# Performance work log

Measured on AMD Instinct MI355X. Metric: run time of the kernel, lower is better.

The kernel has to match this reference:

```python
import jax, jax.numpy as jnp
import numpy as np

# dims (see shape_source)
N, L = 64, 2048          # batch, signal length (l_in)
C1, C2, C3 = 64, 128, 256  # hidden_dims
LAT = 2 * C3             # latent dim: Linear maps L->2 per channel -> C3*2
LD = 64                  # decoder latent spatial length


def conv1d(x, W, b):
    # x: [N,C_in,L], W: [C_out,C_in,3], 'same' padding, stride 1
    y = jax.lax.conv_general_dilated(x, W, window_strides=(1,), padding=((1, 1),),
                                     dimension_numbers=('NCH', 'OIH', 'NCH'))
    return y + b[None, :, None]


def lrelu(v):
    return jnp.where(v > 0, v, 0.01 * v)  # LeakyReLU default slope


def setup_inputs() -> dict:
    key = jax.random.key(0)
    ks = jax.random.split(key, 24)
    r = lambda k, shape, s: (jax.random.normal(k, shape, dtype=jnp.float32) * s)
    inp = {}
    inp['x'] = jax.random.normal(ks[0], (N, 1, L), dtype=jnp.float32)
    # shared encoder (original code reuses the same `modules` for class & style encoders)
    inp['W1'] = r(ks[1], (C1, 1, 3), 0.3);   inp['b1'] = r(ks[2], (C1,), 0.05)
    inp['W2'] = r(ks[3], (C2, C1, 3), 0.08); inp['b2'] = r(ks[4], (C2,), 0.05)
    inp['W3'] = r(ks[5], (C3, C2, 3), 0.06); inp['b3'] = r(ks[6], (C3,), 0.05)
    # heads: Linear(L -> 2) applied on last dim. class_logvar reuses class_mu head (bug in original, kept).
    inp['cm_W'] = r(ks[7], (2, L), 0.02);  inp['cm_b'] = r(ks[8], (2,), 0.05)
    inp['sm_W'] = r(ks[9], (2, L), 0.02);  inp['sm_b'] = r(ks[10], (2,), 0.05)
    inp['sl_W'] = r(ks[11], (2, L), 0.02); inp['sl_b'] = r(ks[12], (2,), 0.05)
    # projections latent -> decoder feature map (minimal repair: original decoder cannot consume a vector)
    inp['pc_W'] = r(ks[13], (C3 * LD, LAT), 0.05); inp['pc_b'] = r(ks[14], (C3 * LD,), 0.05)
    inp['ps_W'] = r(ks[15], (C3 * LD, LAT), 0.05); inp['ps_b'] = r(ks[16], (C3 * LD,), 0.05)
    # shared decoder conv stack (original also shares `modules` between class & style decoders)
    inp['V1'] = r(ks[17], (C2, C3, 3), 0.06); inp['c1'] = r(ks[18], (C2,), 0.05)
    inp['V2'] = r(ks[19], (C1, C2, 3), 0.08); inp['c2'] = r(ks[20], (C1,), 0.05)
    # reparameterization noise (replaces torch.randn_like)
    inp['eps_c'] = jax.random.normal(ks[21], (LAT,), dtype=jnp.float32)
    inp['eps_s'] = jax.random.normal(ks[22], (N, LAT), dtype=jnp.float32)
    return inp


def reference(x, W1, b1, W2, b2, W3, b3, cm_W, cm_b, sm_W, sm_b, sl_W, sl_b,
              pc_W, pc_b, ps_W, ps_b, V1, c1, V2, c2, eps_c, eps_s):
    # ---- encode (shared encoder weights, as in the original module) ----
    h = lrelu(conv1d(x, W1, b1))
    h = lrelu(conv1d(h, W2, b2))
    h = lrelu(conv1d(h, W3, b3))                       # [N, C3, L]
    head = lambda W, b: (jnp.einsum('ncl,dl->ncd', h, W) + b[None, None, :]).reshape(N, -1)
    class_mu = head(cm_W, cm_b)                        # [N, LAT]
    class_logvar = class_mu                            # bug-faithful: class_logvar uses class_mu head
    style_mu = head(sm_W, sm_b)
    style_logvar = head(sl_W, sl_b)
    # ---- accumulate_group_evidence: precision-weighted Gaussian fusion over the batch ----
    prec = jnp.exp(-class_logvar)                      # 1/var, [N, LAT]
    group_var = 1.0 / jnp.sum(prec, axis=0)            # [LAT]
    group_mu = group_var * jnp.sum(class_mu * prec, axis=0)
    group_logvar = jnp.log(group_var)
    # ---- reparameterize ----
    z_c = eps_c * jnp.exp(0.5 * group_logvar) + group_mu       # [LAT]
    z_s = eps_s * jnp.exp(0.5 * style_logvar) + style_mu       # [N, LAT]
    # ---- decode ----
    content = (pc_W @ z_c + pc_b).reshape(1, C3, LD)
    d = jax.nn.relu(conv1d(content, V1, c1))
    d = jax.nn.relu(conv1d(d, V2, c2))                 # [1, C1, LD]
    source = jnp.mean(d, axis=0).reshape(-1)           # [C1*LD] fixed observation kernel
    m = (z_s @ ps_W.T + ps_b[None, :]).reshape(N, C3, LD)
    m = jax.nn.relu(conv1d(m, V1, c1))
    m = jax.nn.relu(conv1d(m, V2, c2)).reshape(N, -1)  # [N, C1*LD]
    # F.conv_transpose1d(media, source) with stride 1 == full 1D convolution
    out = jax.vmap(lambda mi: jnp.convolve(mi, source, mode='full'))(m)
    return out.reshape(N, 1, -1)                       # [N, 1, 2*C1*LD - 1]
```

## Files before the change

### kernel.cpp

```cpp
#include <hip/hip_runtime.h>
#include <math.h>


using short8  = __attribute__((ext_vector_type(8))) short;
using floatx4 = __attribute__((ext_vector_type(4))) float;

__device__ __forceinline__ float lrelu_s(float v, float slope) {
  return v > 0.f ? v : slope * v;
}
__device__ __forceinline__ unsigned short bf16_rne(float f) {
  unsigned u = __float_as_uint(f);
  u += 0x7FFFu + ((u >> 16) & 1u);
  return (unsigned short)(u >> 16);
}
__device__ __forceinline__ float bf16_to_f(unsigned short h) {
  return __uint_as_float(((unsigned)h) << 16);
}

__global__ __launch_bounds__(256) void prep_weights_kernel(
    const float* __restrict__ W2, const float* __restrict__ W3,
    unsigned short* __restrict__ w2hi, unsigned short* __restrict__ w2lo,
    unsigned short* __restrict__ w3hi, unsigned short* __restrict__ w3lo)
{
  int id = blockIdx.x * 256 + threadIdx.x;
  if (id < 24576) {
    int t = id % 3, rem = id / 3;
    int ci = rem % 64, co = rem / 64;
    float w = W2[id];
    unsigned short hi = bf16_rne(w);
    unsigned short lo = bf16_rne(w - bf16_to_f(hi));
    int o = (t * 128 + co) * 64 + ci;
    w2hi[o] = hi; w2lo[o] = lo;
  } else if (id < 24576 + 98304) {
    int i3 = id - 24576;
    int t = i3 % 3, rem = i3 / 3;
    int ci = rem % 128, co = rem / 128;
    float w = W3[i3];
    unsigned short hi = bf16_rne(w);
    unsigned short lo = bf16_rne(w - bf16_to_f(hi));
    int o = (t * 256 + co) * 128 + ci;
    w3hi[o] = hi; w3lo[o] = lo;
  }
}

template<int CIN, int COUT, int LLEN>
__global__ __launch_bounds__(256) void convlv(
    const float* __restrict__ in, const float* __restrict__ W,
    const float* __restrict__ bias, float* __restrict__ out, float slope)
{
  const int n    = blockIdx.x;
  const int wv   = __builtin_amdgcn_readfirstlane(threadIdx.x >> 6);
  const int c0   = blockIdx.y * 32 + wv * 8;
  const int lane = threadIdx.x & 63;
  const int lbase = blockIdx.z * 256 + lane * 4;
  const float* inn = in + (size_t)n * CIN * LLEN;

  const bool bm = (lbase == 0);
  const bool bp = (lbase + 4 == LLEN);
  unsigned o0 = (unsigned)lbase;
  unsigned om = (unsigned)lbase - 1u + (bm ? 1u : 0u);
  unsigned op = (unsigned)lbase + 4u - (bp ? 1u : 0u);

  float acc[8][4];
  #pragma unroll
  for (int q = 0; q < 8; ++q) {
    float b = bias[c0 + q];
    #pragma unroll
    for (int e = 0; e < 4; ++e) acc[q][e] = b;
  }
  for (int ci = 0; ci < CIN; ++ci) {
    float4 x  = *(const float4*)(inn + o0);
    float xm0 = inn[om]; if (bm) xm0 = 0.f;
    float xp3 = inn[op]; if (bp) xp3 = 0.f;
    o0 += LLEN; om += LLEN; op += LLEN;
    float w[8][3];
    #pragma unroll
    for (int q = 0; q < 8; ++q) {
      const float* wp = W + ((size_t)(c0 + q) * CIN + ci) * 3;
      w[q][0] = wp[0]; w[q][1] = wp[1]; w[q][2] = wp[2];
    }
    #pragma unroll
    for (int q = 0; q < 8; ++q) {
      acc[q][0] = fmaf(xm0, w[q][0], fmaf(x.x, w[q][1], fmaf(x.y, w[q][2], acc[q][0])));
      acc[q][1] = fmaf(x.x, w[q][0], fmaf(x.y, w[q][1], fmaf(x.z, w[q][2], acc[q][1])));
      acc[q][2] = fmaf(x.y, w[q][0], fmaf(x.z, w[q][1], fmaf(x.w, w[q][2], acc[q][2])));
      acc[q][3] = fmaf(x.z, w[q][0], fmaf(x.w, w[q][1], fmaf(xp3, w[q][2], acc[q][3])));
    }
  }
  #pragma unroll
  for (int q = 0; q < 8; ++q) {
    float4 r;
    r.x = lrelu_s(acc[q][0], slope);
    r.y = lrelu_s(acc[q][1], slope);
    r.z = lrelu_s(acc[q][2], slope);
    r.w = lrelu_s(acc[q][3], slope);
    *(float4*)(out + ((size_t)n * COUT + c0 + q) * LLEN + lbase) = r;
  }
}

template<int CIN, int COUT, bool HEADS>
__global__ __launch_bounds__(256, 3) void conv_mfma(
    const float* __restrict__ in, const unsigned short* __restrict__ Whi,
    const unsigned short* __restrict__ Wlo, const float* __restrict__ bias,
    float* __restrict__ out, float* __restrict__ hpart,
    const float* __restrict__ cmW, const float* __restrict__ smW,
    const float* __restrict__ slW)
{
  __shared__ unsigned short smem[22176];
  const int tid  = threadIdx.x;
  const int n    = blockIdx.x;
  const int coT  = blockIdx.y;
  const int lt   = blockIdx.z;
  const int l0   = lt * 128;
  const int wid  = __builtin_amdgcn_readfirstlane(tid >> 6);
  const int wm   = wid >> 1, wn = wid & 1;
  const int lane = tid & 63;
  const int l16  = lane & 15, lk = lane >> 4;
  const float* inn = in + (size_t)n * CIN * 2048;

  if (HEADS) {
    for (int idx = tid; idx < 768; idx += 256) {
      int h6 = idx >> 7, l = idx & 127;
      const float* src = (h6 < 2) ? cmW : (h6 < 4 ? smW : slW);
      ((float*)(smem + 20640))[idx] = src[(h6 & 1) * 2048 + l0 + l];
    }
  }

  floatx4 acc[4][4];
  #pragma unroll
  for (int mf = 0; mf < 4; ++mf) {
    #pragma unroll
    for (int r = 0; r < 4; ++r) {
      float bv = bias[coT * 128 + wm * 64 + mf * 16 + lk * 4 + r];
      #pragma unroll
      for (int nf = 0; nf < 4; ++nf) acc[mf][nf][r] = bv;
    }
  }

  const int s_steps = CIN / 32;
  for (int s = 0; s < s_steps; ++s) {
    const int ci0 = s * 32;
    __syncthreads();
    {
      const int l4 = tid >> 3;
      const int cb = tid & 7;
      #pragma unroll
      for (int p = 0; p < 4; ++p) {
        int c = cb + 8 * p;
        const float4 v4 = *(const float4*)(inn + (size_t)(ci0 + c) * 2048 + l0 + l4 * 4);
        #pragma unroll
        for (int e = 0; e < 4; ++e) {
          float v = (&v4.x)[e];
          unsigned short hi = bf16_rne(v);
          unsigned short lo = bf16_rne(v - bf16_to_f(hi));
          int r = l4 * 4 + e + 1;
          smem[r * 40 + c]        = hi;
          smem[5200 + r * 40 + c] = lo;
        }
      }
      if (tid < 64) {
        int ce = tid & 31, e = tid >> 5;
        int le = e ? (l0 + 128) : (l0 - 1);
        float v = 0.f;
        if (le >= 0 && le < 2048) v = inn[(size_t)(ci0 + ce) * 2048 + le];
        unsigned short hi = bf16_rne(v);
        unsigned short lo = bf16_rne(v - bf16_to_f(hi));
        int r = e ? 129 : 0;
        smem[r * 40 + ce]        = hi;
        smem[5200 + r * 40 + ce] = lo;
      }
    }
    #pragma unroll
    for (int t = 0; t < 3; ++t) {
      if (t > 0) __syncthreads();
      {
        int co  = tid >> 1;
        int h16 = (tid & 1) * 16;
        const size_t gb = ((size_t)(t * COUT) + coT * 128 + co) * CIN + ci0 + h16;
        #pragma unroll
        for (int p = 0; p < 2; ++p) {
          short8 hi = *(const short8*)(Whi + gb + 8 * p);
          short8 lo = *(const short8*)(Wlo + gb + 8 * p);
          *(short8*)(smem + 10400 + co * 40 + h16 + 8 * p) = hi;
          *(short8*)(smem + 15520 + co * 40 + h16 + 8 * p) = lo;
        }
      }
      __syncthreads();
      short8 ahi[4], alo[4];
      #pragma unroll
      for (int mf = 0; mf < 4; ++mf) {
        int off = (wm * 64 + mf * 16 + l16) * 40 + lk * 8;
        ahi[mf] = *(const short8*)(smem + 10400 + off);
        alo[mf] = *(const short8*)(smem + 15520 + off);
      }
      #pragma unroll
      for (int nf = 0; nf < 4; ++nf) {
        int rr  = wn * 64 + nf * 16 + l16 + t;
        int off = rr * 40 + lk * 8;
        short8 bhi = *(const short8*)(smem + off);
        short8 blo = *(const short8*)(smem + 5200 + off);
        #pragma unroll
        for (int mf = 0; mf < 4; ++mf) {
          acc[mf][nf] = __builtin_amdgcn_mfma_f32_16x16x32_bf16(ahi[mf], bhi, acc[mf][nf], 0, 0, 0);
          acc[mf][nf] = __builtin_amdgcn_mfma_f32_16x16x32_bf16(ahi[mf], blo, acc[mf][nf], 0, 0, 0);
          acc[mf][nf] = __builtin_amdgcn_mfma_f32_16x16x32_bf16(alo[mf], bhi, acc[mf][nf], 0, 0, 0);
        }
      }
    }
  }

  if (!HEADS) {
    #pragma unroll
    for (int mf = 0; mf < 4; ++mf)
      #pragma unroll
      for (int nf = 0; nf < 4; ++nf)
        #pragma unroll
        for (int r = 0; r < 4; ++r) {
          float v = lrelu_s(acc[mf][nf][r], 0.01f);
          out[((size_t)n * COUT + coT * 128 + wm * 64 + mf * 16 + lk * 4 + r) * 2048
              + l0 + wn * 64 + nf * 16 + l16] = v;
        }
  } else {
    float* H = (float*)smem;
    const float* hwl = (const float*)(smem + 20640);
    #pragma unroll
    for (int p = 0; p < 2; ++p) {
      __syncthreads();
      if (wm == p) {
        #pragma unroll
        for (int mf = 0; mf < 4; ++mf)
          #pragma unroll
          for (int nf = 0; nf < 4; ++nf)
            #pragma unroll
            for (int r = 0; r < 4; ++r) {
              float v = lrelu_s(acc[mf][nf][r], 0.01f);
              H[(mf * 16 + lk * 4 + r) * 132 + wn * 64 + nf * 16 + l16] = v;
            }
      }
      __syncthreads();
      int co = tid >> 2, q = tid & 3;
      float sacc[6] = {0.f, 0.f, 0.f, 0.f, 0.f, 0.f};
      #pragma unroll
      for (int e4 = 0; e4 < 8; ++e4) {
        float4 hv = *(const float4*)(H + co * 132 + q * 32 + e4 * 4);
        #pragma unroll
        for (int ee = 0; ee < 4; ++ee) {
          float v = (&hv.x)[ee];
          int ll = q * 32 + e4 * 4 + ee;
          #pragma unroll
          for (int h6 = 0; h6 < 6; ++h6)
            sacc[h6] = fmaf(v, hwl[h6 * 128 + ll], sacc[h6]);
        }
      }
      #pragma unroll
      for (int h6 = 0; h6 < 6; ++h6) {
        sacc[h6] += __shfl_xor(sacc[h6], 1);
        sacc[h6] += __shfl_xor(sacc[h6], 2);
      }
      if (q == 0) {
        int j = (coT * 128 + p * 64 + co) * 2;
        #pragma unroll
        for (int hd = 0; hd < 3; ++hd) {
          float2 st = make_float2(sacc[hd * 2], sacc[hd * 2 + 1]);
          *(float2*)(hpart + ((size_t)((lt * 64 + n) * 3 + hd)) * 512 + j) = st;
        }
      }
    }
  }
}

__global__ __launch_bounds__(256) void head_combine_kernel(
    const float* __restrict__ hpart, float* __restrict__ cm,
    float* __restrict__ smv, float* __restrict__ sl)
{
  int n = blockIdx.x;
  int j = threadIdx.x * 2;
  float2 s0 = {0.f, 0.f}, s1 = {0.f, 0.f}, s2 = {0.f, 0.f};
  for (int ltt = 0; ltt < 16; ++ltt) {
    const float* base = hpart + ((size_t)((ltt * 64 + n) * 3)) * 512 + j;
    float2 a = *(const float2*)(base);
    float2 b = *(const float2*)(base + 512);
    float2 c = *(const float2*)(base + 1024);
    s0.x += a.x; s0.y += a.y;
    s1.x += b.x; s1.y += b.y;
    s2.x += c.x; s2.y += c.y;
  }
  *(float2*)(cm  + n * 512 + j) = s0;
  *(float2*)(smv + n * 512 + j) = s1;
  *(float2*)(sl  + n * 512 + j) = s2;
}

__global__ __launch_bounds__(256) void group_reparam_kernel(
    const float* __restrict__ cm, const float* __restrict__ sm,
    const float* __restrict__ sl,
    const float* __restrict__ cmB, const float* __restrict__ smB,
    const float* __restrict__ slB,
    const float* __restrict__ eps_c, const float* __restrict__ eps_s,
    float* __restrict__ zc, float* __restrict__ zs)
{
  const int j = blockIdx.x * 256 + threadIdx.x;
  if (j >= 512) return;
  const int d = j & 1;
  const float cb = cmB[d], sb = smB[d], lb = slB[d];
  float sp = 0.f, smp = 0.f;
  for (int n = 0; n < 64; ++n) {
    float mu = cm[n * 512 + j] + cb;
    float p  = expf(-mu);
    sp += p;
    smp = fmaf(mu, p, smp);
  }
  float gv  = 1.f / sp;
  float gmu = gv * smp;
  zc[j] = eps_c[j] * sqrtf(gv) + gmu;
  for (int n = 0; n < 64; ++n)
    zs[n * 512 + j] = eps_s[n * 512 + j] * expf(0.5f * (sl[n * 512 + j] + lb))
                      + (sm[n * 512 + j] + sb);
}

__global__ __launch_bounds__(256) void matvec_content_kernel(
    const float* __restrict__ pcW, const float* __restrict__ pcb,
    const float* __restrict__ zc, float* __restrict__ content)
{
  const int r    = blockIdx.x * 4 + (threadIdx.x >> 6);
  const int lane = threadIdx.x & 63;
  const float* row = pcW + (size_t)r * 512;
  float s = 0.f;
  #pragma unroll
  for (int i = 0; i < 8; ++i) {
    int k = lane + i * 64;
    s = fmaf(row[k], zc[k], s);
  }
  for (int off = 32; off > 0; off >>= 1) s += __shfl_down(s, off, 64);
  if (lane == 0) content[r] = s + pcb[r];
}

__global__ __launch_bounds__(256) void gemm_m0_kernel(
    const float* __restrict__ psW, const float* __restrict__ psb,
    const float* __restrict__ zs, float* __restrict__ m0)
{
  __shared__ float wrow[16][512];
  const int r0 = blockIdx.x * 16;
  for (int idx = threadIdx.x; idx < 2048; idx += 256)
    ((float4*)wrow)[idx] = ((const float4*)(psW + (size_t)r0 * 512))[idx];
  __syncthreads();
  const int rs = threadIdx.x >> 6;
  const int nn = threadIdx.x & 63;
  const float* zr = zs + nn * 512;
  float a0 = 0.f, a1 = 0.f, a2 = 0.f, a3 = 0.f;
  for (int k = 0; k < 512; k += 4) {
    float4 z  = *(const float4*)(zr + k);
    float4 w0 = *(const float4*)(&wrow[rs * 4 + 0][k]);
    float4 w1 = *(const float4*)(&wrow[rs * 4 + 1][k]);
    float4 w2 = *(const float4*)(&wrow[rs * 4 + 2][k]);
    float4 w3 = *(const float4*)(&wrow[rs * 4 + 3][k]);
    a0 = fmaf(z.x, w0.x, fmaf(z.y, w0.y, fmaf(z.z, w0.z, fmaf(z.w, w0.w, a0))));
    a1 = fmaf(z.x, w1.x, fmaf(z.y, w1.y, fmaf(z.z, w1.z, fmaf(z.w, w1.w, a1))));
    a2 = fmaf(z.x, w2.x, fmaf(z.y, w2.y, fmaf(z.z, w2.z, fmaf(z.w, w2.w, a2))));
    a3 = fmaf(z.x, w3.x, fmaf(z.y, w3.y, fmaf(z.z, w3.z, fmaf(z.w, w3.w, a3))));
  }
  const int rb = r0 + rs * 4;
  m0[(size_t)nn * 16384 + rb + 0] = a0 + psb[rb + 0];
  m0[(size_t)nn * 16384 + rb + 1] = a1 + psb[rb + 1];
  m0[(size_t)nn * 16384 + rb + 2] = a2 + psb[rb + 2];
  m0[(size_t)nn * 16384 + rb + 3] = a3 + psb[rb + 3];
}

template<int CIN, int COUT>
__global__ __launch_bounds__(256) void convs64(
    const float* __restrict__ in0, const float* __restrict__ inC,
    const float* __restrict__ W, const float* __restrict__ bias,
    float* __restrict__ out0, float* __restrict__ outC)
{
  const int n    = blockIdx.x;
  const int wv   = __builtin_amdgcn_readfirstlane(threadIdx.x >> 6);
  const int c0   = blockIdx.y * 32 + wv * 8;
  const int lane = threadIdx.x & 63;
  const float* inn = (n < 64) ? (in0 + (size_t)n * CIN * 64) : inC;
  float* outp      = (n < 64) ? (out0 + (size_t)n * COUT * 64) : outC;

  float acc[8];
  #pragma unroll
  for (int q = 0; q < 8; ++q) acc[q] = bias[c0 + q];

  unsigned o = (unsigned)lane;
  for (int ci = 0; ci < CIN; ++ci) {
    float x0 = inn[o];
    o += 64;
    float xm = __shfl_up(x0, 1);   if (lane == 0)  xm = 0.f;
    float xp = __shfl_down(x0, 1); if (lane == 63) xp = 0.f;
    float w[8][3];
    #pragma unroll
    for (int q = 0; q < 8; ++q) {
      const float* wp = W + ((size_t)(c0 + q) * CIN + ci) * 3;
      w[q][0] = wp[0]; w[q][1] = wp[1]; w[q][2] = wp[2];
    }
    #pragma unroll
    for (int q = 0; q < 8; ++q)
      acc[q] = fmaf(xm, w[q][0], fmaf(x0, w[q][1], fmaf(xp, w[q][2], acc[q])));
  }
  #pragma unroll
  for (int q = 0; q < 8; ++q)
    outp[(size_t)(c0 + q) * 64 + lane] = acc[q] > 0.f ? acc[q] : 0.f;
}

__global__ __launch_bounds__(256) void final_conv_part_kernel(
    const float* __restrict__ m2, const float* __restrict__ src,
    float* __restrict__ part)
{
  __shared__ float s_src[4096];
  __shared__ float s_m[1024];
  const int n  = blockIdx.x;
  const int J0 = blockIdx.z * 1024;
  for (int i = threadIdx.x; i < 4096; i += 256) s_src[i] = src[i];
  for (int i = threadIdx.x; i < 1024; i += 256) s_m[i] = m2[(size_t)n * 4096 + J0 + i];
  __syncthreads();

  const int k0 = blockIdx.y * 2048 + threadIdx.x * 8;
  int jlo = k0 - 4095; if (jlo < J0) jlo = J0;
  int jhi = k0 + 7;    if (jhi > J0 + 1023) jhi = J0 + 1023;

  float acc[8];
  #pragma unroll
  for (int ii = 0; ii < 8; ++ii) acc[ii] = 0.f;

  float Wr[8];
  #pragma unroll
  for (int p = 0; p < 8; ++p) {
    int d  = k0 + p - jlo;
    int dc = d & 4095;
    float v = s_src[dc];
    Wr[p] = (d == dc) ? v : 0.f;
  }
  int j = jlo;
  for (; j + 7 <= jhi; j += 8) {
    #pragma unroll
    for (int s = 0; s < 8; ++s) {
      float mj = s_m[j + s - J0];
      #pragma unroll
      for (int ii = 0; ii < 8; ++ii)
        acc[ii] = fmaf(mj, Wr[(ii - s) & 7], acc[ii]);
      int d  = k0 - (j + s) - 1;
      int dc = d < 0 ? 0 : d;
      float nv = s_src[dc];
      if (d < 0) nv = 0.f;
      Wr[(7 - s) & 7] = nv;
    }
  }
  for (; j <= jhi; ++j) {
    float mj = s_m[j - J0];
    #pragma unroll
    for (int ii = 0; ii < 8; ++ii) {
      int d  = k0 + ii - j;
      int dc = d & 4095;
      float sv = s_src[dc];
      if (d != dc) sv = 0.f;
      acc[ii] = fmaf(mj, sv, acc[ii]);
    }
  }
  float* po = part + ((size_t)(blockIdx.z * 64 + n)) * 8192 + k0;
  #pragma unroll
  for (int ii = 0; ii < 8; ++ii) po[ii] = acc[ii];
}

__global__ void combine_kernel(const float* __restrict__ part,
                               float* __restrict__ out) {
  int i = blockIdx.x * 256 + threadIdx.x;
  if (i >= 64 * 8191) return;
  int n = i / 8191, k = i - n * 8191;
  float s = 0.f;
  #pragma unroll
  for (int js = 0; js < 4; ++js)
    s += part[((size_t)(js * 64 + n)) * 8192 + k];
  out[i] = s;
}

extern "C" void kernel_launch(void* const* d_in, const int* in_sizes, int n_in,
                              void* d_out, int out_size, void* d_ws, size_t ws_size,
                              hipStream_t stream) {
  const float* x    = (const float*)d_in[0];
  const float* W1   = (const float*)d_in[1];
  const float* b1   = (const float*)d_in[2];
  const float* W2   = (const float*)d_in[3];
  const float* b2   = (const float*)d_in[4];
  const float* W3   = (const float*)d_in[5];
  const float* b3   = (const float*)d_in[6];
  const float* cmW  = (const float*)d_in[7];
  const float* cmB  = (const float*)d_in[8];
  const float* smW  = (const float*)d_in[9];
  const float* smB  = (const float*)d_in[10];
  const float* slW  = (const float*)d_in[11];
  const float* slB  = (const float*)d_in[12];
  const float* pcW  = (const float*)d_in[13];
  const float* pcb  = (const float*)d_in[14];
  const float* psW  = (const float*)d_in[15];
  const float* psb  = (const float*)d_in[16];
  const float* V1   = (const float*)d_in[17];
  const float* c1   = (const float*)d_in[18];
  const float* V2   = (const float*)d_in[19];
  const float* c2   = (const float*)d_in[20];
  const float* epsc = (const float*)d_in[21];
  const float* epss = (const float*)d_in[22];
  float* out = (float*)d_out;

  float* ws = (float*)d_ws;
  float* h1 = ws;
  float* h2 = h1 + 8388608;
  float* hpart   = h1;
  float* cm      = h1 + 1572864;
  float* smh     = h1 + 1605632;
  float* slh     = h1 + 1638400;
  float* zc      = h1 + 1671168;
  float* zs      = h1 + 1671680;
  float* content = h1 + 1704448;
  float* d1s     = h1 + 1720832;
  float* srcb    = h1 + 1729024;
  float* m0      = h1 + 1733120;
  float* m1      = h1 + 2781696;
  float* m2      = h1 + 3305984;
  float* part    = h1 + 3568128;
  unsigned short* wsp  = (unsigned short*)d_out;
  unsigned short* w2hi = wsp;
  unsigned short* w2lo = wsp + 24576;
  unsigned short* w3hi = wsp + 49152;
  unsigned short* w3lo = wsp + 147456;
  (void)ws_size; (void)in_sizes; (void)n_in; (void)out_size;

  prep_weights_kernel<<<480, 256, 0, stream>>>(W2, W3, w2hi, w2lo, w3hi, w3lo);

  convlv<1, 64, 2048><<<dim3(64, 2, 8), 256, 0, stream>>>(x, W1, b1, h1, 0.01f);
  conv_mfma<64, 128, false><<<dim3(64, 1, 16), 256, 0, stream>>>(
      h1, w2hi, w2lo, b2, h2, nullptr, cmW, smW, slW);
  conv_mfma<128, 256, true><<<dim3(64, 2, 16), 256, 0, stream>>>(
      h2, w3hi, w3lo, b3, nullptr, hpart, cmW, smW, slW);
  head_combine_kernel<<<64, 256, 0, stream>>>(hpart, cm, smh, slh);

  group_reparam_kernel<<<2, 256, 0, stream>>>(cm, smh, slh, cmB, smB, slB,
                                              epsc, epss, zc, zs);

  matvec_content_kernel<<<4096, 256, 0, stream>>>(pcW, pcb, zc, content);
  gemm_m0_kernel<<<1024, 256, 0, stream>>>(psW, psb, zs, m0);

  convs64<256, 128><<<dim3(65, 4), 256, 0, stream>>>(m0, content, V1, c1, m1, d1s);
  convs64<128, 64><<<dim3(65, 2), 256, 0, stream>>>(m1, d1s, V2, c2, m2, srcb);

  final_conv_part_kernel<<<dim3(64, 4, 4), 256, 0, stream>>>(m2, srcb, part);
  combine_kernel<<<2048, 256, 0, stream>>>(part, out);
}
```

Measured before the change: 621.2 us.

## Stage activations as fp32 in LDS and split to bf16 hi/lo at fragment load

The conv MFMA kernel now copies input activations into LDS as raw fp32 rows with float4 stores, instead of splitting each value into bf16 hi/lo and scattering them with transposed 16-bit stores. The split into hi/lo bf16 now happens when each wave builds its B fragment, using the packed v_cvt_pk_bf16_f32 instruction. The head-weight staging moves after the main loop so its LDS region can be reused, and the occupancy hint rises from 3 to 4 blocks per CU. The cost is repeated conversion work per fragment read (each activation is converted for every t and wn), plus strided LDS reads of 4-byte values.

```diff
diff --git a/kernel.cpp b/kernel.cpp
--- a/kernel.cpp
+++ b/kernel.cpp
@@ -15,6 +15,11 @@
 }
 __device__ __forceinline__ float bf16_to_f(unsigned short h) {
   return __uint_as_float(((unsigned)h) << 16);
+}
+__device__ __forceinline__ unsigned cvt_pk_bf16(float a, float b) {
+  unsigned r;
+  asm("v_cvt_pk_bf16_f32 %0, %1, %2" : "=v"(r) : "v"(a), "v"(b));
+  return r;
 }
 
 __global__ __launch_bounds__(256) void prep_weights_kernel(
@@ -99,14 +104,19 @@
 }
 
 template<int CIN, int COUT, bool HEADS>
-__global__ __launch_bounds__(256, 3) void conv_mfma(
+__global__ __launch_bounds__(256, 4) void conv_mfma(
     const float* __restrict__ in, const unsigned short* __restrict__ Whi,
     const unsigned short* __restrict__ Wlo, const float* __restrict__ bias,
     float* __restrict__ out, float* __restrict__ hpart,
     const float* __restrict__ cmW, const float* __restrict__ smW,
     const float* __restrict__ slW)
 {
-  __shared__ unsigned short smem[22176];
+  __shared__ float4 smem4[2400];
+  char* smem = (char*)smem4;
+  float*          Bf  = (float*)smem;
+  unsigned short* Ahi = (unsigned short*)(smem + 17920);
+  unsigned short* Alo = (unsigned short*)(smem + 28160);
+
   const int tid  = threadIdx.x;
   const int n    = blockIdx.x;
   const int coT  = blockIdx.y;
@@ -118,14 +128,6 @@
   const int l16  = lane & 15, lk = lane >> 4;
   const float* inn = in + (size_t)n * CIN * 2048;
 
-  if (HEADS) {
-    for (int idx = tid; idx < 768; idx += 256) {
-      int h6 = idx >> 7, l = idx & 127;
-      const float* src = (h6 < 2) ? cmW : (h6 < 4 ? smW : slW);
-      ((float*)(smem + 20640))[idx] = src[(h6 & 1) * 2048 + l0 + l];
-    }
-  }
-
   floatx4 acc[4][4];
   #pragma unroll
   for (int mf = 0; mf < 4; ++mf) {
@@ -142,32 +144,21 @@
     const int ci0 = s * 32;
     __syncthreads();
     {
-      const int l4 = tid >> 3;
-      const int cb = tid & 7;
-      #pragma unroll
-      for (int p = 0; p < 4; ++p) {
-        int c = cb + 8 * p;
-        const float4 v4 = *(const float4*)(inn + (size_t)(ci0 + c) * 2048 + l0 + l4 * 4);
-        #pragma unroll
-        for (int e = 0; e < 4; ++e) {
-          float v = (&v4.x)[e];
-          unsigned short hi = bf16_rne(v);
-          unsigned short lo = bf16_rne(v - bf16_to_f(hi));
-          int r = l4 * 4 + e + 1;
-          smem[r * 40 + c]        = hi;
-          smem[5200 + r * 40 + c] = lo;
-        }
+      const int ci = tid >> 3, f4 = tid & 7;
+      const float* rowp = inn + (size_t)(ci0 + ci) * 2048 + l0;
+      float* ldsrow = Bf + ci * 140;
+      #pragma unroll
+      for (int it = 0; it < 4; ++it) {
+        int c4 = f4 + 8 * it;
+        float4 v = *(const float4*)(rowp + 4 * c4);
+        *(float4*)(ldsrow + 4 + 4 * c4) = v;
       }
       if (tid < 64) {
-        int ce = tid & 31, e = tid >> 5;
-        int le = e ? (l0 + 128) : (l0 - 1);
+        int ce = tid & 31, side = tid >> 5;
+        int lg = side ? (l0 + 128) : (l0 - 1);
         float v = 0.f;
-        if (le >= 0 && le < 2048) v = inn[(size_t)(ci0 + ce) * 2048 + le];
-        unsigned short hi = bf16_rne(v);
-        unsigned short lo = bf16_rne(v - bf16_to_f(hi));
-        int r = e ? 129 : 0;
-        smem[r * 40 + ce]        = hi;
-        smem[5200 + r * 40 + ce] = lo;
+        if (lg >= 0 && lg < 2048) v = inn[(size_t)(ci0 + ce) * 2048 + lg];
+        Bf[ce * 140 + (side ? 132 : 3)] = v;
       }
     }
     #pragma unroll
@@ -177,33 +168,38 @@
         int co  = tid >> 1;
         int h16 = (tid & 1) * 16;
         const size_t gb = ((size_t)(t * COUT) + coT * 128 + co) * CIN + ci0 + h16;
-        #pragma unroll
-        for (int p = 0; p < 2; ++p) {
-          short8 hi = *(const short8*)(Whi + gb + 8 * p);
-          short8 lo = *(const short8*)(Wlo + gb + 8 * p);
-          *(short8*)(smem + 10400 + co * 40 + h16 + 8 * p) = hi;
-          *(short8*)(smem + 15520 + co * 40 + h16 + 8 * p) = lo;
-        }
+        *(short8*)(Ahi + co * 40 + h16)     = *(const short8*)(Whi + gb);
+        *(short8*)(Ahi + co * 40 + h16 + 8) = *(const short8*)(Whi + gb + 8);
+        *(short8*)(Alo + co * 40 + h16)     = *(const short8*)(Wlo + gb);
+        *(short8*)(Alo + co * 40 + h16 + 8) = *(const short8*)(Wlo + gb + 8);
       }
       __syncthreads();
       short8 ahi[4], alo[4];
       #pragma unroll
       for (int mf = 0; mf < 4; ++mf) {
         int off = (wm * 64 + mf * 16 + l16) * 40 + lk * 8;
-        ahi[mf] = *(const short8*)(smem + 10400 + off);
-        alo[mf] = *(const short8*)(smem + 15520 + off);
+        ahi[mf] = *(const short8*)(Ahi + off);
+        alo[mf] = *(const short8*)(Alo + off);
       }
       #pragma unroll
       for (int nf = 0; nf < 4; ++nf) {
-        int rr  = wn * 64 + nf * 16 + l16 + t;
-        int off = rr * 40 + lk * 8;
-        short8 bhi = *(const short8*)(smem + off);
-        short8 blo = *(const short8*)(smem + 5200 + off);
+        const float* bp = Bf + (lk * 8) * 140 + (wn * 64 + nf * 16 + l16 + t + 3);
+        union { short8 s; unsigned u[4]; } bh, bl;
+        #pragma unroll
+        for (int jp = 0; jp < 4; ++jp) {
+          float a = bp[(2 * jp) * 140];
+          float b = bp[(2 * jp + 1) * 140];
+          unsigned hi = cvt_pk_bf16(a, b);
+          float ha = __uint_as_float(hi << 16);
+          float hb = __uint_as_float(hi & 0xffff0000u);
+          bh.u[jp] = hi;
+          bl.u[jp] = cvt_pk_bf16(a - ha, b - hb);
+        }
         #pragma unroll
         for (int mf = 0; mf < 4; ++mf) {
-          acc[mf][nf] = __builtin_amdgcn_mfma_f32_16x16x32_bf16(ahi[mf], bhi, acc[mf][nf], 0, 0, 0);
-          acc[mf][nf] = __builtin_amdgcn_mfma_f32_16x16x32_bf16(ahi[mf], blo, acc[mf][nf], 0, 0, 0);
-          acc[mf][nf] = __builtin_amdgcn_mfma_f32_16x16x32_bf16(alo[mf], bhi, acc[mf][nf], 0, 0, 0);
+          acc[mf][nf] = __builtin_amdgcn_mfma_f32_16x16x32_bf16(ahi[mf], bh.s, acc[mf][nf], 0, 0, 0);
+          acc[mf][nf] = __builtin_amdgcn_mfma_f32_16x16x32_bf16(ahi[mf], bl.s, acc[mf][nf], 0, 0, 0);
+          acc[mf][nf] = __builtin_amdgcn_mfma_f32_16x16x32_bf16(alo[mf], bh.s, acc[mf][nf], 0, 0, 0);
         }
       }
     }
@@ -221,8 +217,14 @@
               + l0 + wn * 64 + nf * 16 + l16] = v;
         }
   } else {
-    float* H = (float*)smem;
-    const float* hwl = (const float*)(smem + 20640);
+    float* H   = (float*)smem;
+    float* hwl = (float*)(smem + 33792);
+    __syncthreads();
+    for (int idx = tid; idx < 768; idx += 256) {
+      int h6 = idx >> 7, l = idx & 127;
+      const float* src = (h6 < 2) ? cmW : (h6 < 4 ? smW : slW);
+      hwl[idx] = src[(h6 & 1) * 2048 + l0 + l];
+    }
     #pragma unroll
     for (int p = 0; p < 2; ++p) {
       __syncthreads();
```

New measurement: 709.1 us. 1.14x slower.
